# Kernel optimization log

Measured on AMD Instinct MI355X. Metric: run time of the kernel, lower is better.

Reference implementation:

```python
import jax, jax.numpy as jnp
import numpy as np

# static config (matches init_kwargs)
B, Q, D, H, L, P, V, T = 4, 32, 512, 8, 4, 4, 12000, 16
HD = D // H                      # attn_feat_dim = d_model / n_heads
TS = [2048, 1024, 512, 256]      # temporal_shapes (1-D feature pyramid)
LS = [0, 2048, 3072, 3584]       # level_start_index
S = sum(TS)


def setup_inputs() -> dict:
    key = jax.random.key(0)
    ks = jax.random.split(key, 20)
    f = jnp.float32
    def n(k, shape, s=0.02):
        return jax.random.normal(k, shape, dtype=f) * s
    return dict(
        seq_tokens=jax.random.randint(ks[0], (B * Q, T), 0, V),
        decoder_hidden_states=n(ks[1], (B, Q, D), 1.0),
        reference_points=jax.random.uniform(ks[2], (B, Q, 1), dtype=f),
        enc=n(ks[3], (B, S, D), 1.0),
        valid_ratios=jnp.ones((B, L), dtype=f),
        mask_flatten=jnp.zeros((B, S), dtype=bool),
        temporal_shapes=jnp.array(TS, dtype=jnp.int32),
        level_start_index=jnp.array(LS, dtype=jnp.int32),
        embed_W=jax.random.uniform(ks[4], (V, D), dtype=f, minval=-0.1, maxval=0.1),
        logit_W=jax.random.uniform(ks[5], (V, D), dtype=f, minval=-0.1, maxval=0.1),
        logit_b=jnp.zeros((V,), f),
        Wih=n(ks[6], (4 * D, 3 * D)),   # LSTM weight_ih (no bias), gate order i,f,g,o
        Whh=n(ks[7], (4 * D, D)),       # LSTM weight_hh
        value_W=n(ks[8], (D, D)), value_b=jnp.zeros((D,), f),
        off_W=n(ks[9], (H * L * P, 2 * D)), off_b=n(ks[10], (H * L * P,), 0.5),
        aw_W=n(ks[11], (H * L * P, 2 * D)), aw_b=jnp.zeros((H * L * P,), f),
        ctx_W=n(ks[12], (D, HD)), ctx_b=jnp.zeros((D,), f),
        hs_W=n(ks[13], (D, D)), hs_b=jnp.zeros((D,), f),
        alpha_W=n(ks[14], (1, D)), alpha_b=jnp.zeros((1,), f),
    )


def _forward(seq_tokens, decoder_hidden_states, reference_points, enc, valid_ratios,
             mask_flatten, temporal_shapes, level_start_index,
             embed_W, logit_W, logit_b, Wih, Whh, value_W, value_b,
             off_W, off_b, aw_W, aw_b, ctx_W, ctx_b, hs_W, hs_b, alpha_W, alpha_b):
    ts = [int(t) for t in np.asarray(temporal_shapes)]
    ls = [int(s) for s in np.asarray(level_start_index)]
    query = decoder_hidden_states            # (B, Q, D)
    BQ = B * Q
    # prepare_for_captioning: ref (B,Q,1) -> (B,Q,L,1) scaled by valid_ratios
    refp = reference_points[:, :, None, :] * valid_ratios[:, None, :, None]
    # value projection + padding mask
    value = jnp.where(mask_flatten[..., None], 0.0, enc @ value_W.T + value_b).reshape(B, S, H, HD)
    v_levels = [value[:, ls[l]:ls[l] + ts[l]].transpose(0, 2, 1, 3) for l in range(L)]  # (B,H,Tl,HD)
    ts_f = jnp.asarray(ts, dtype=query.dtype)

    def sample_level(v_l, loc, Tl):
        # 1-D linear interpolation, align_corners=False, zero padding (grid_sample style)
        # v_l: (B,H,Tl,HD); loc: (B,Q,H,P) normalized in [0,1]
        x = loc * Tl - 0.5
        x0 = jnp.floor(x)
        w = (x - x0)[..., None].transpose(0, 2, 1, 3, 4)   # (B,H,Q,P,1)
        i0 = x0.astype(jnp.int32)
        def gather(i):
            m = ((i >= 0) & (i < Tl))[..., None].astype(v_l.dtype).transpose(0, 2, 1, 3, 4)
            idx = jnp.clip(i, 0, Tl - 1).transpose(0, 2, 1, 3).reshape(B, H, Q * P)
            g = jnp.take_along_axis(v_l, idx[..., None], axis=2)  # (B,H,Q*P,HD)
            return g.reshape(B, H, Q, P, HD) * m
        return gather(i0) * (1.0 - w) + gather(i0 + 1) * w        # (B,H,Q,P,HD)

    def step(carry, tok):
        h, c = carry                                              # (BQ, D) each
        # TemporalMSDA query = cat(prev_h, query)
        hs_in = jnp.concatenate([h.reshape(B, Q, D), query], axis=2)       # (B,Q,2D)
        off = (hs_in @ off_W.T + off_b).reshape(B, Q, H, L, P)
        aw = jax.nn.softmax((hs_in @ aw_W.T + aw_b).reshape(B, Q, H, L * P), axis=-1)
        loc = refp[:, :, None, :, :] + off / ts_f[None, None, None, :, None]  # (B,Q,H,L,P)
        sampled = jnp.stack([sample_level(v_levels[l], loc[..., l, :], ts[l])
                             for l in range(L)], axis=3).reshape(B, H, Q, L * P, HD)
        weighted = sampled * aw.transpose(0, 2, 1, 3)[..., None]  # per-point MSDA-weighted values
        ctx = weighted.transpose(0, 2, 1, 3, 4).reshape(BQ, H, L * P, HD)
        # tanh additive attention over the L*P sampled points (per head)
        attn = ctx @ ctx_W.T + ctx_b                              # (BQ,H,LP,D)
        attn_h = (h @ hs_W.T + hs_b)[:, None, None, :]
        dot = (jnp.tanh(attn + attn_h) @ alpha_W.T + alpha_b)[..., 0]  # (BQ,H,LP)
        wgt = jax.nn.softmax(dot, axis=-1)
        attn_res = jnp.einsum('bhp,bhpd->bhd', wgt, ctx).reshape(BQ, D)
        # LSTM cell (bias=False), torch gate order i,f,g,o
        x = jnp.concatenate([embed_W[tok], attn_res, query.reshape(BQ, D)], axis=1)
        gates = x @ Wih.T + h @ Whh.T
        gi, gf, gg, go = jnp.split(gates, 4, axis=1)
        c2 = jax.nn.sigmoid(gf) * c + jax.nn.sigmoid(gi) * jnp.tanh(gg)
        h2 = jax.nn.sigmoid(go) * jnp.tanh(c2)
        return (h2, c2), jax.nn.log_softmax(h2 @ logit_W.T + logit_b, axis=-1)

    h0 = jnp.zeros((BQ, D), dtype=query.dtype)
    _, outs = jax.lax.scan(step, (h0, h0), seq_tokens[:, :-1].T)   # (T-1, BQ, V)
    return outs.transpose(1, 0, 2).reshape(B, Q, T - 1, V)


def reference(seq_tokens, decoder_hidden_states, reference_points, enc, valid_ratios,
              mask_flatten, temporal_shapes, level_start_index,
              embed_W, logit_W, logit_b, Wih, Whh, value_W, value_b,
              off_W, off_b, aw_W, aw_b, ctx_W, ctx_b, hs_W, hs_b, alpha_W, alpha_b):
    return _forward(seq_tokens, decoder_hidden_states, reference_points, enc, valid_ratios,
                    mask_flatten, temporal_shapes, level_start_index,
                    embed_W, logit_W, logit_b, Wih, Whh, value_W, value_b,
                    off_W, off_b, aw_W, aw_b, ctx_W, ctx_b, hs_W, hs_b, alpha_W, alpha_b)
```

## Files before the change

kernel.cpp:

```cpp
#include <hip/hip_runtime.h>

#define B_ 4
#define Q_ 32
#define D_ 512
#define H_ 8
#define L_ 4
#define P_ 4
#define V_ 12000
#define T_ 16
#define HD_ 64
#define S_ 3840
#define BQ_ 128
#define NSTEP 15
#define NSLAB 94

typedef __attribute__((ext_vector_type(8))) short short8;
typedef __attribute__((ext_vector_type(4))) float f32x4;

__device__ inline unsigned short f2bf(float x) {
  union { float f; unsigned u; } v; v.f = x;
  unsigned u = v.u;
  unsigned r = (u + 0x7fffu + ((u >> 16) & 1u)) >> 16;
  return (unsigned short)r;
}
__device__ inline float bf2f(unsigned short b) {
  union { unsigned u; float f; } v; v.u = ((unsigned)b) << 16; return v.f;
}
__device__ inline float fast_tanh(float x) {
  x = fminf(fmaxf(x, -15.f), 15.f);
  float e = __expf(2.f * x);
  return (e - 1.f) / (e + 1.f);
}
__device__ inline float sigmoidf_(float x) { return 1.f / (1.f + __expf(-x)); }

#define APAD 40
struct SmemGemm {
  unsigned short As0[128 * APAD], Bs0[128 * APAD];
  unsigned short As1[128 * APAD], Bs1[128 * APAD];
};
struct SmemGemmS {
  unsigned short As[128 * APAD], Bs[128 * APAD];
};
struct SmemSample {
  float ctx_s[16][HD_];
  unsigned short ctxbf[16][72];
  float aw_s[16];
  float wgt_s[16];
  float wred[4][16];
};

__device__ inline short8 cvt8(float4 v0, float4 v1) {
  short8 p;
  p[0] = (short)f2bf(v0.x); p[1] = (short)f2bf(v0.y);
  p[2] = (short)f2bf(v0.z); p[3] = (short)f2bf(v0.w);
  p[4] = (short)f2bf(v1.x); p[5] = (short)f2bf(v1.y);
  p[6] = (short)f2bf(v1.z); p[7] = (short)f2bf(v1.w);
  return p;
}

__device__ inline void mfma_step(const unsigned short* As, const unsigned short* Bs,
                                 f32x4 acc[4][4], int wm, int wn, int lane) {
  int r15 = lane & 15, koct = (lane >> 4) * 8;
  short8 a[4], b[4];
#pragma unroll
  for (int mf = 0; mf < 4; mf++)
    a[mf] = *(const short8*)(As + (wm * 64 + mf * 16 + r15) * APAD + koct);
#pragma unroll
  for (int nf = 0; nf < 4; nf++)
    b[nf] = *(const short8*)(Bs + (wn * 64 + nf * 16 + r15) * APAD + koct);
#pragma unroll
  for (int mf = 0; mf < 4; mf++)
#pragma unroll
    for (int nf = 0; nf < 4; nf++)
      acc[mf][nf] = __builtin_amdgcn_mfma_f32_16x16x32_bf16(a[mf], b[nf], acc[mf][nf], 0, 0, 0);
}

template <int NT, class FA, class FB>
__device__ inline void gemm_pipe(FA loadA, FB loadB, SmemGemm& sm,
                                 f32x4 acc[4][4], int wm, int wn, int lane, int tid) {
  int r = tid >> 2, ko = (tid & 3) * 8;
  short8 a0, a1, b0, b1;
  loadA(0, a0, a1); loadB(0, b0, b1);
#pragma unroll
  for (int t = 0; t < NT; t++) {
    unsigned short* As = (t & 1) ? sm.As1 : sm.As0;
    unsigned short* Bs = (t & 1) ? sm.Bs1 : sm.Bs0;
    *(short8*)(As + r * APAD + ko) = a0;
    *(short8*)(As + (r + 64) * APAD + ko) = a1;
    *(short8*)(Bs + r * APAD + ko) = b0;
    *(short8*)(Bs + (r + 64) * APAD + ko) = b1;
    short8 na0, na1, nb0, nb1;
    if (t + 1 < NT) { loadA(t + 1, na0, na1); loadB(t + 1, nb0, nb1); }
    __syncthreads();
    mfma_step(As, Bs, acc, wm, wn, lane);
    if (t + 1 < NT) { a0 = na0; a1 = na1; b0 = nb0; b1 = nb1; }
  }
}

template <int NT, class FA, class FB>
__device__ inline void gemm_simple(FA loadA, FB loadB, SmemGemmS& sm,
                                   f32x4 acc[4][4], int wm, int wn, int lane, int tid) {
  int r = tid >> 2, ko = (tid & 3) * 8;
#pragma unroll 2
  for (int t = 0; t < NT; t++) {
    short8 a0, a1, b0, b1;
    loadA(t, a0, a1); loadB(t, b0, b1);
    *(short8*)(sm.As + r * APAD + ko) = a0;
    *(short8*)(sm.As + (r + 64) * APAD + ko) = a1;
    *(short8*)(sm.Bs + r * APAD + ko) = b0;
    *(short8*)(sm.Bs + (r + 64) * APAD + ko) = b1;
    __syncthreads();
    mfma_step(sm.As, sm.Bs, acc, wm, wn, lane);
    __syncthreads();
  }
}

__device__ inline void mfma_epilogue(float* __restrict__ out, int ldo, int m0, int n0,
                                     int Nmax, const float* __restrict__ bias,
                                     const unsigned char* __restrict__ mask,
                                     const float* __restrict__ base,
                                     f32x4 acc[4][4], int wm, int wn, int lane) {
  int rb = (lane >> 4) * 4, cb = lane & 15;
#pragma unroll
  for (int nf = 0; nf < 4; nf++) {
    int col = n0 + wn * 64 + nf * 16 + cb;
    if (col >= Nmax) continue;
    float bv = bias ? bias[col] : 0.f;
#pragma unroll
    for (int mf = 0; mf < 4; mf++) {
#pragma unroll
      for (int j = 0; j < 4; j++) {
        int row = m0 + wm * 64 + mf * 16 + rb + j;
        float v = acc[mf][nf][j] + bv;
        if (base) v += base[(size_t)row * ldo + col];
        if (mask && mask[row]) v = 0.f;
        out[(size_t)row * ldo + col] = v;
      }
    }
  }
}

__device__ inline void mfma_epilogue_bf16b(unsigned short* __restrict__ out, int ldo,
                                           int m0, int n0,
                                           const float* __restrict__ bias,
                                           const unsigned char* __restrict__ mask,
                                           f32x4 acc[4][4], int wm, int wn, int lane) {
  int rb = (lane >> 4) * 4, cb = lane & 15;
#pragma unroll
  for (int nf = 0; nf < 4; nf++) {
    int col = n0 + wn * 64 + nf * 16 + cb;
    float bv = bias ? bias[col] : 0.f;
#pragma unroll
    for (int mf = 0; mf < 4; mf++) {
#pragma unroll
      for (int j = 0; j < 4; j++) {
        int row = m0 + wm * 64 + mf * 16 + rb + j;
        float v = acc[mf][nf][j] + bv;
        if (mask && mask[row]) v = 0.f;
        out[(size_t)row * ldo + col] = f2bf(v);
      }
    }
  }
}

__device__ inline void mfma_epilogue_bf16(unsigned short* __restrict__ out, int ldo, int n0,
                                          f32x4 acc[4][4], int wm, int wn, int lane) {
  int rb = (lane >> 4) * 4, cb = lane & 15;
#pragma unroll
  for (int nf = 0; nf < 4; nf++) {
    int col = n0 + wn * 64 + nf * 16 + cb;
#pragma unroll
    for (int mf = 0; mf < 4; mf++) {
#pragma unroll
      for (int j = 0; j < 4; j++) {
        int row = wm * 64 + mf * 16 + rb + j;
        out[(size_t)row * ldo + col] = f2bf(acc[mf][nf][j]);
      }
    }
  }
}

#define ACC_INIT f32x4 acc[4][4]; { f32x4 z = {0.f,0.f,0.f,0.f}; \
  _Pragma("unroll") for (int i_=0;i_<4;i_++) _Pragma("unroll") for (int j_=0;j_<4;j_++) acc[i_][j_]=z; }


__global__ __launch_bounds__(256) void k_prep(const float* __restrict__ logitW,
    const float* __restrict__ Wih, const float* __restrict__ Whh,
    const float* __restrict__ offW, const float* __restrict__ awW,
    const float* __restrict__ hsW, const float* __restrict__ valueW,
    const float* __restrict__ query, const float* __restrict__ ctxW,
    const int* __restrict__ seq, const float* __restrict__ embedW,
    unsigned short* __restrict__ logitWbf, unsigned short* __restrict__ Wihbf,
    unsigned short* __restrict__ Whhbf, unsigned short* __restrict__ offWbf,
    unsigned short* __restrict__ awWbf, unsigned short* __restrict__ hsWbf,
    unsigned short* __restrict__ valueWbf, unsigned short* __restrict__ qbf,
    unsigned short* __restrict__ ctxWbf, unsigned short* __restrict__ hall,
    float* __restrict__ c0, unsigned short* __restrict__ xembbf) {
  int gi = blockIdx.x * 256 + threadIdx.x;
  const int e0 = 1536000, e1 = e0 + 786432, e2 = e1 + 262144, e3 = e2 + 32768,
            e4 = e3 + 32768, e5 = e4 + 65536, e6 = e5 + 65536, e7 = e6 + 16384;
  const int e8 = e7 + 16384, e9 = e8 + 8192, e10 = e9 + 245760;
  if (gi < e7) {
    const float* src; unsigned short* dst; int lo, dsti;
    if (gi < e0)      { src = logitW; dst = logitWbf; lo = gi; dsti = lo; }
    else if (gi < e1) {
      src = Wih; dst = Wihbf; lo = gi - e0;
      int row = lo / 384, c4 = lo - row * 384;
      int g = row >> 9, d = row & 511, n = d >> 5, rr = d & 31;
      dsti = (n * 128 + g * 32 + rr) * 384 + c4;
    }
    else if (gi < e2) {
      src = Whh; dst = Whhbf; lo = gi - e1;
      int row = lo >> 7, c4 = lo & 127;
      int g = row >> 9, d = row & 511, n = d >> 5, rr = d & 31;
      dsti = (n * 128 + g * 32 + rr) * 128 + c4;
    }
    else if (gi < e3) { src = offW;   dst = offWbf;   lo = gi - e2; dsti = lo; }
    else if (gi < e4) { src = awW;    dst = awWbf;    lo = gi - e3; dsti = lo; }
    else if (gi < e5) { src = hsW;    dst = hsWbf;    lo = gi - e4; dsti = lo; }
    else if (gi < e6) { src = valueW; dst = valueWbf; lo = gi - e5; dsti = lo; }
    else              { src = query;  dst = qbf;      lo = gi - e6; dsti = lo; }
    float4 v = ((const float4*)src)[lo];
    ushort4 o;
    o.x = f2bf(v.x); o.y = f2bf(v.y); o.z = f2bf(v.z); o.w = f2bf(v.w);
    ((ushort4*)dst)[dsti] = o;
  } else if (gi < e8) {
    int i = gi - e7;
    ushort4 z4; z4.x = 0; z4.y = 0; z4.z = 0; z4.w = 0;
    ((ushort4*)hall)[i] = z4;
    float4 z = {0.f, 0.f, 0.f, 0.f};
    ((float4*)c0)[i] = z;
  } else if (gi < e9) {
    int i = gi - e8;
    float4 v = ((const float4*)ctxW)[i];
    ushort4 o;
    o.x = f2bf(v.x); o.y = f2bf(v.y); o.z = f2bf(v.z); o.w = f2bf(v.w);
    ((ushort4*)ctxWbf)[i] = o;
  } else if (gi < e10) {
    int i = gi - e9;
    int row = i >> 7, d4 = i & 127;
    int t = row >> 7, bq = row & 127;
    int tok = seq[bq * T_ + t];
    float4 v = ((const float4*)embedW)[(size_t)tok * 128 + d4];
    ushort4 o;
    o.x = f2bf(v.x); o.y = f2bf(v.y); o.z = f2bf(v.z); o.w = f2bf(v.w);
    ((ushort4*)xembbf)[(size_t)row * 128 + d4] = o;
  }
}

__global__ __launch_bounds__(256) void k_value(const float* __restrict__ enc,
    const unsigned short* __restrict__ valueWbf, const float* __restrict__ valueb,
    const unsigned char* __restrict__ mask, unsigned short* __restrict__ value) {
  __shared__ SmemGemmS sm;
  int blk = blockIdx.x;
  int xcd = blk & 7, j = blk >> 3;
  int m0 = (xcd * 15 + (j >> 2)) * 128, n0 = (j & 3) * 128;
  int tid = threadIdx.x;
  int lane = tid & 63, w = tid >> 6, wm = w >> 1, wn = w & 1;
  int r = tid >> 2, ko = (tid & 3) * 8;
  ACC_INIT;
  gemm_simple<16>(
    [&](int t, short8& x, short8& y) {
      const float4* s0 = (const float4*)(enc + (size_t)(m0 + r) * 512 + t * 32 + ko);
      const float4* s1 = (const float4*)(enc + (size_t)(m0 + r + 64) * 512 + t * 32 + ko);
      x = cvt8(s0[0], s0[1]); y = cvt8(s1[0], s1[1]);
    },
    [&](int t, short8& x, short8& y) {
      x = *(const short8*)(valueWbf + (size_t)(n0 + r) * 512 + t * 32 + ko);
      y = *(const short8*)(valueWbf + (size_t)(n0 + r + 64) * 512 + t * 32 + ko);
    },
    sm, acc, wm, wn, lane, tid);
  mfma_epilogue_bf16b(value, 512, m0, n0, valueb, mask, acc, wm, wn, lane);
}

__global__ __launch_bounds__(256) void k_qg(const unsigned short* __restrict__ qbf,
    const unsigned short* __restrict__ offWbf, const float* __restrict__ offb,
    const unsigned short* __restrict__ awWbf, const float* __restrict__ awb,
    float* __restrict__ off_base, float* __restrict__ aw_base,
    const unsigned short* __restrict__ xembbf,
    const unsigned short* __restrict__ Wihbf, unsigned short* __restrict__ gates_base) {
  __shared__ SmemGemmS sm;
  int blk = blockIdx.x;
  int tid = threadIdx.x;
  int lane = tid & 63, w = tid >> 6, wm = w >> 1, wn = w & 1;
  int r = tid >> 2, ko = (tid & 3) * 8;
  if (blk < 2) {
    const unsigned short* Bw = blk ? awWbf : offWbf;
    const float* bias = blk ? awb : offb;
    float* out = blk ? aw_base : off_base;
    ACC_INIT;
    gemm_simple<16>(
      [&](int t, short8& x, short8& y) {
        x = *(const short8*)(qbf + (size_t)r * 512 + t * 32 + ko);
        y = *(const short8*)(qbf + (size_t)(r + 64) * 512 + t * 32 + ko);
      },
      [&](int t, short8& x, short8& y) {
        x = *(const short8*)(Bw + (size_t)r * 1024 + 512 + t * 32 + ko);
        y = *(const short8*)(Bw + (size_t)(r + 64) * 1024 + 512 + t * 32 + ko);
      },
      sm, acc, wm, wn, lane, tid);
    mfma_epilogue(out, 128, 0, 0, 128, bias, nullptr, nullptr, acc, wm, wn, lane);
  } else {
    int g = blk - 2;
    int xcd = g & 7, j = g >> 3;
    int n0 = (xcd * 2 + (j >= 15)) * 128;
    int st = (j >= 15) ? (j - 15) : j;
    const unsigned short* xa = xembbf + (size_t)(st * 128) * 512;
    ACC_INIT;
    gemm_simple<32>(
      [&](int t, short8& x, short8& y) {
        const unsigned short* src = (t < 16) ? xa : qbf;
        int kk = (t < 16) ? t * 32 : (t - 16) * 32;
        x = *(const short8*)(src + (size_t)r * 512 + kk + ko);
        y = *(const short8*)(src + (size_t)(r + 64) * 512 + kk + ko);
      },
      [&](int t, short8& x, short8& y) {
        int kk = (t < 16) ? t * 32 : 1024 + (t - 16) * 32;
        x = *(const short8*)(Wihbf + (size_t)(n0 + r) * 1536 + kk + ko);
        y = *(const short8*)(Wihbf + (size_t)(n0 + r + 64) * 1536 + kk + ko);
      },
      sm, acc, wm, wn, lane, tid);
    mfma_epilogue_bf16(gates_base + (size_t)st * 128 * 2048, 2048, n0, acc, wm, wn, lane);
  }
}

__global__ __launch_bounds__(256) void k_sample(const unsigned short* __restrict__ value,
    const float* __restrict__ off_src, const float* __restrict__ aw_src,
    const float* __restrict__ hp_src, int hstride,
    const float* __restrict__ refp, const float* __restrict__ vrat,
    const unsigned short* __restrict__ ctxWbf, const float* __restrict__ ctxb,
    const float* __restrict__ alphaW, const float* __restrict__ alphab,
    unsigned short* __restrict__ attnbf) {
  __shared__ SmemSample sm;
  int blk = blockIdx.x;
  int bq = blk >> 3, h = blk & 7;
  int b = bq >> 5;
  int tid = threadIdx.x;
  int lane = tid & 63, wid = tid >> 6;

  if (tid < 16) {
    float v = aw_src[bq * 128 + h * 16 + tid];
    float m = v;
#pragma unroll
    for (int o = 8; o; o >>= 1) m = fmaxf(m, __shfl_xor(m, o, 16));
    float e = __expf(v - m);
    float s = e;
#pragma unroll
    for (int o = 8; o; o >>= 1) s += __shfl_xor(s, o, 16);
    sm.aw_s[tid] = e / s;
  }
  __syncthreads();

  {
    const int TSv[4] = {2048, 1024, 512, 256};
    const int LSv[4] = {0, 2048, 3072, 3584};
    float ref = refp[bq];
    int hd = tid & 63;
#pragma unroll
    for (int pp = 0; pp < 4; pp++) {
      int p = pp * 4 + (tid >> 6);
      int l = p >> 2;
      int Tl = TSv[l];
      float off = off_src[bq * 128 + h * 16 + p];
      float loc = ref * vrat[b * L_ + l] + off / (float)Tl;
      float x = loc * (float)Tl - 0.5f;
      float x0 = floorf(x);
      float wf = x - x0;
      int i0 = (int)x0;
      const unsigned short* vb = value + ((size_t)(b * S_ + LSv[l]) * D_) + h * HD_ + hd;
      float v0 = (i0 >= 0 && i0 < Tl) ? bf2f(vb[(size_t)i0 * D_]) : 0.f;
      float v1 = (i0 + 1 >= 0 && i0 + 1 < Tl) ? bf2f(vb[(size_t)(i0 + 1) * D_]) : 0.f;
      float cv = (v0 * (1.f - wf) + v1 * wf) * sm.aw_s[p];
      sm.ctx_s[p][hd] = cv;
      sm.ctxbf[p][hd] = f2bf(cv);
    }
  }
  __syncthreads();

  {
    int r15 = lane & 15, koct = (lane >> 4) * 8;
    int rb = (lane >> 4) * 4, cb = lane & 15;
    short8 a0 = *(const short8*)(&sm.ctxbf[r15][koct]);
    short8 a1 = *(const short8*)(&sm.ctxbf[r15][32 + koct]);
    float part0 = 0.f, part1 = 0.f, part2 = 0.f, part3 = 0.f;
#pragma unroll
    for (int nf = 0; nf < 8; nf++) {
      int d0 = wid * 128 + nf * 16;
      const unsigned short* bp = ctxWbf + (size_t)(d0 + r15) * 64;
      short8 b0 = *(const short8*)(bp + koct);
      short8 b1 = *(const short8*)(bp + 32 + koct);
      f32x4 acc = {0.f, 0.f, 0.f, 0.f};
      acc = __builtin_amdgcn_mfma_f32_16x16x32_bf16(a0, b0, acc, 0, 0, 0);
      acc = __builtin_amdgcn_mfma_f32_16x16x32_bf16(a1, b1, acc, 0, 0, 0);
      int d = d0 + cb;
      float add = ctxb[d] + hp_src[(size_t)hstride * bq + d];
      float al = alphaW[d];
      part0 += al * fast_tanh(acc[0] + add);
      part1 += al * fast_tanh(acc[1] + add);
      part2 += al * fast_tanh(acc[2] + add);
      part3 += al * fast_tanh(acc[3] + add);
    }
#pragma unroll
    for (int o = 8; o; o >>= 1) {
      part0 += __shfl_xor(part0, o, 16);
      part1 += __shfl_xor(part1, o, 16);
      part2 += __shfl_xor(part2, o, 16);
      part3 += __shfl_xor(part3, o, 16);
    }
    if (cb == 0) {
      sm.wred[wid][rb + 0] = part0;
      sm.wred[wid][rb + 1] = part1;
      sm.wred[wid][rb + 2] = part2;
      sm.wred[wid][rb + 3] = part3;
    }
  }
  __syncthreads();
  if (tid < 16) {
    float v = sm.wred[0][tid] + sm.wred[1][tid] + sm.wred[2][tid] + sm.wred[3][tid] + alphab[0];
    float m = v;
#pragma unroll
    for (int o = 8; o; o >>= 1) m = fmaxf(m, __shfl_xor(m, o, 16));
    float e = __expf(v - m);
    float s = e;
#pragma unroll
    for (int o = 8; o; o >>= 1) s += __shfl_xor(s, o, 16);
    sm.wgt_s[tid] = e / s;
  }
  __syncthreads();
  if (tid < 64) {
    float a = 0.f;
#pragma unroll
    for (int pi = 0; pi < 16; pi++) a += sm.wgt_s[pi] * sm.ctx_s[pi][tid];
    attnbf[bq * D_ + h * HD_ + tid] = f2bf(a);
  }
}

__global__ __launch_bounds__(256) void k_lstm_gemm(
    const unsigned short* __restrict__ attnbf, const unsigned short* __restrict__ hcur,
    const unsigned short* __restrict__ Wihbf, const unsigned short* __restrict__ Whhbf,
    float* __restrict__ gpart) {
  __shared__ SmemGemm sm;
  int tid = threadIdx.x;
  int lane = tid & 63, w = tid >> 6, wm = w >> 1, wn = w & 1;
  int r = tid >> 2, ko = (tid & 3) * 8;
  int n0 = blockIdx.x * 128;
  int kc = blockIdx.y;
  const unsigned short* Asrc = (kc < 2) ? (attnbf + kc * 256) : (hcur + (kc - 2) * 256);
  const unsigned short* Bsrc = (kc < 2) ? (Wihbf + (size_t)n0 * 1536 + 512 + kc * 256)
                                        : (Whhbf + (size_t)n0 * 512 + (kc - 2) * 256);
  int ldB = (kc < 2) ? 1536 : 512;
  ACC_INIT;
  gemm_pipe<8>(
    [&](int t, short8& x, short8& y) {
      x = *(const short8*)(Asrc + (size_t)r * 512 + t * 32 + ko);
      y = *(const short8*)(Asrc + (size_t)(r + 64) * 512 + t * 32 + ko);
    },
    [&](int t, short8& x, short8& y) {
      x = *(const short8*)(Bsrc + (size_t)r * ldB + t * 32 + ko);
      y = *(const short8*)(Bsrc + (size_t)(r + 64) * ldB + t * 32 + ko);
    },
    sm, acc, wm, wn, lane, tid);
  mfma_epilogue(gpart + (size_t)kc * 262144, 2048, 0, n0, 2048,
                nullptr, nullptr, nullptr, acc, wm, wn, lane);
}

__global__ __launch_bounds__(256) void k_cell(const float* __restrict__ gpart,
    const unsigned short* __restrict__ gbase_t,
    const float* __restrict__ c, float* __restrict__ cn, unsigned short* __restrict__ hout) {
  int idx = blockIdx.x * 256 + threadIdx.x;
  int bq = idx >> 9, d = idx & 511;
  int n = d >> 5, rr = d & 31;
  size_t rowoff = (size_t)bq * 2048 + n * 128 + rr;
  float g4[4];
#pragma unroll
  for (int gate = 0; gate < 4; gate++) {
    size_t off = rowoff + gate * 32;
    float s = bf2f(gbase_t[off]);
    s += gpart[off] + gpart[262144 + off] + gpart[2 * 262144 + off] + gpart[3 * 262144 + off];
    g4[gate] = s;
  }
  float cc = c[idx];
  float c2 = sigmoidf_(g4[1]) * cc + sigmoidf_(g4[0]) * fast_tanh(g4[2]);
  float h2 = sigmoidf_(g4[3]) * fast_tanh(c2);
  cn[idx] = c2;
  hout[idx] = f2bf(h2);
}

__global__ __launch_bounds__(256) void k_pre(const unsigned short* __restrict__ hbf,
    const unsigned short* __restrict__ offWbf, const unsigned short* __restrict__ awWbf,
    const unsigned short* __restrict__ hsWbf, const float* __restrict__ hsb,
    const float* __restrict__ off_base, const float* __restrict__ aw_base,
    float* __restrict__ offo, float* __restrict__ awo, float* __restrict__ hpo) {
  __shared__ SmemGemm sm;
  int blk = blockIdx.x;
  const unsigned short* Bw; const float* bias; const float* base;
  float* out; int ldkB, n0, ldo;
  if (blk == 0)      { Bw = offWbf; bias = nullptr; base = off_base; out = offo; ldkB = 1024; n0 = 0; ldo = 128; }
  else if (blk == 1) { Bw = awWbf;  bias = nullptr; base = aw_base;  out = awo;  ldkB = 1024; n0 = 0; ldo = 128; }
  else { Bw = hsWbf; bias = hsb; base = nullptr; out = hpo; ldkB = 512; n0 = (blk - 2) * 128; ldo = 512; }
  int tid = threadIdx.x;
  int lane = tid & 63, w = tid >> 6, wm = w >> 1, wn = w & 1;
  int r = tid >> 2, ko = (tid & 3) * 8;
  ACC_INIT;
  gemm_pipe<16>(
    [&](int t, short8& x, short8& y) {
      x = *(const short8*)(hbf + (size_t)r * 512 + t * 32 + ko);
      y = *(const short8*)(hbf + (size_t)(r + 64) * 512 + t * 32 + ko);
    },
    [&](int t, short8& x, short8& y) {
      x = *(const short8*)(Bw + (size_t)(n0 + r) * ldkB + t * 32 + ko);
      y = *(const short8*)(Bw + (size_t)(n0 + r + 64) * ldkB + t * 32 + ko);
    },
    sm, acc, wm, wn, lane, tid);
  mfma_epilogue(out, ldo, 0, n0, ldo, bias, nullptr, base, acc, wm, wn, lane);
}

__global__ __launch_bounds__(256) void k_logits_big(
    const unsigned short* __restrict__ logitWbf, const float* __restrict__ logitb,
    const unsigned short* __restrict__ hall, float* __restrict__ outp,
    float* __restrict__ m_sb, float* __restrict__ s_sb) {
  __shared__ SmemGemm sm;
  __shared__ float mred[128][2], sred[128][2];
  int blk = blockIdx.x;
  int swz = (blk & 7) * 177 + (blk >> 3);
  if (swz >= NSLAB * NSTEP) return;
  int slab = swz / NSTEP, t = swz % NSTEP;
  int n0 = slab * 128;
  int tid = threadIdx.x;
  int lane = tid & 63, w = tid >> 6, wm = w >> 1, wn = w & 1;
  int r = tid >> 2, ko = (tid & 3) * 8;
  const unsigned short* hn = hall + (size_t)(t + 1) * 65536;
  bool ok0 = (n0 + r) < V_, ok1 = (n0 + r + 64) < V_;
  ACC_INIT;
  gemm_pipe<16>(
    [&](int tt, short8& x, short8& y) {
      x = *(const short8*)(hn + (size_t)r * 512 + tt * 32 + ko);
      y = *(const short8*)(hn + (size_t)(r + 64) * 512 + tt * 32 + ko);
    },
    [&](int tt, short8& x, short8& y) {
      short8 z = {0, 0, 0, 0, 0, 0, 0, 0};
      x = ok0 ? *(const short8*)(logitWbf + (size_t)(n0 + r) * 512 + tt * 32 + ko) : z;
      y = ok1 ? *(const short8*)(logitWbf + (size_t)(n0 + r + 64) * 512 + tt * 32 + ko) : z;
    },
    sm, acc, wm, wn, lane, tid);
  int rb = (lane >> 4) * 4, cb = lane & 15;
#pragma unroll
  for (int mf = 0; mf < 4; mf++) {
#pragma unroll
    for (int j = 0; j < 4; j++) {
      int row = wm * 64 + mf * 16 + rb + j;
      float vv[4];
      float mx = -3.4e38f;
#pragma unroll
      for (int nf = 0; nf < 4; nf++) {
        int col = n0 + wn * 64 + nf * 16 + cb;
        bool ok = col < V_;
        float v = ok ? (acc[mf][nf][j] + logitb[col]) : -3.4e38f;
        if (ok) outp[((size_t)row * NSTEP + t) * V_ + col] = v;
        vv[nf] = v;
        mx = fmaxf(mx, v);
      }
#pragma unroll
      for (int o = 8; o; o >>= 1) mx = fmaxf(mx, __shfl_xor(mx, o, 16));
      float sme = 0.f;
#pragma unroll
      for (int nf = 0; nf < 4; nf++) sme += (vv[nf] > -3.0e38f) ? __expf(vv[nf] - mx) : 0.f;
#pragma unroll
      for (int o = 8; o; o >>= 1) sme += __shfl_xor(sme, o, 16);
      if (cb == 0) { mred[row][wn] = mx; sred[row][wn] = sme; }
    }
  }
  __syncthreads();
  if (tid < 128) {
    float m0 = mred[tid][0], m1 = mred[tid][1];
    float M = fmaxf(m0, m1);
    float Ssum = sred[tid][0] * __expf(m0 - M) + sred[tid][1] * __expf(m1 - M);
    m_sb[((size_t)t * 128 + tid) * 96 + slab] = M;
    s_sb[((size_t)t * 128 + tid) * 96 + slab] = Ssum;
  }
}

__global__ __launch_bounds__(256) void k_out_all(const float* __restrict__ m_sb,
    const float* __restrict__ s_sb, float* __restrict__ outp) {
  __shared__ float ms[NSLAB], ss[NSLAB];
  __shared__ float lse_s;
  int blk = blockIdx.x;
  int t = blk >> 7, row = blk & 127;
  int tid = threadIdx.x;
  size_t pbase = ((size_t)t * 128 + row) * 96;
  if (tid < NSLAB) { ms[tid] = m_sb[pbase + tid]; ss[tid] = s_sb[pbase + tid]; }
  __syncthreads();
  if (tid < 64) {
    float m = -3.4e38f, s = 0.f;
    for (int i = tid; i < NSLAB; i += 64) {
      float mi = ms[i], si = ss[i];
      float M = fmaxf(m, mi);
      s = s * __expf(m - M) + si * __expf(mi - M);
      m = M;
    }
#pragma unroll
    for (int o = 32; o; o >>= 1) {
      float mo = __shfl_xor(m, o, 64), so = __shfl_xor(s, o, 64);
      float M = fmaxf(m, mo);
      s = s * __expf(m - M) + so * __expf(mo - M);
      m = M;
    }
    if (tid == 0) lse_s = m + __logf(s);
  }
  __syncthreads();
  float lse = lse_s;
  float4* op = (float4*)(outp + ((size_t)row * NSTEP + t) * V_);
  for (int i = tid; i < V_ / 4; i += 256) {
    float4 v = op[i];
    v.x -= lse; v.y -= lse; v.z -= lse; v.w -= lse;
    op[i] = v;
  }
}

extern "C" void kernel_launch(void* const* d_in, const int* in_sizes, int n_in,
                              void* d_out, int out_size, void* d_ws, size_t ws_size,
                              hipStream_t stream) {
  const int* seq             = (const int*)d_in[0];
  const float* query         = (const float*)d_in[1];
  const float* refp          = (const float*)d_in[2];
  const float* enc           = (const float*)d_in[3];
  const float* vrat          = (const float*)d_in[4];
  const unsigned char* mask  = (const unsigned char*)d_in[5];
  const float* embedW        = (const float*)d_in[8];
  const float* logitW        = (const float*)d_in[9];
  const float* logitb        = (const float*)d_in[10];
  const float* Wih           = (const float*)d_in[11];
  const float* Whh           = (const float*)d_in[12];
  const float* valueW        = (const float*)d_in[13];
  const float* valueb        = (const float*)d_in[14];
  const float* offW          = (const float*)d_in[15];
  const float* offb          = (const float*)d_in[16];
  const float* awW           = (const float*)d_in[17];
  const float* awb           = (const float*)d_in[18];
  const float* ctxW          = (const float*)d_in[19];
  const float* ctxb          = (const float*)d_in[20];
  const float* hsW           = (const float*)d_in[21];
  const float* hsb           = (const float*)d_in[22];
  const float* alphaW        = (const float*)d_in[23];
  const float* alphab        = (const float*)d_in[24];

  char* wp = (char*)d_ws;
  auto alloc_f = [&](size_t n) { float* p = (float*)wp; wp += ((n * 4 + 255) / 256) * 256; return p; };
  auto alloc_u = [&](size_t n) { unsigned short* p = (unsigned short*)wp; wp += ((n * 2 + 255) / 256) * 256; return p; };

  float* gpart   = alloc_f((size_t)4 * BQ_ * 2048);
  float* hproj   = alloc_f((size_t)BQ_ * D_);
  float* offo    = alloc_f((size_t)BQ_ * 128);
  float* awo     = alloc_f((size_t)BQ_ * 128);
  float* off_base= alloc_f((size_t)BQ_ * 128);
  float* aw_base = alloc_f((size_t)BQ_ * 128);
  float* c0      = alloc_f((size_t)BQ_ * D_);
  float* c1      = alloc_f((size_t)BQ_ * D_);
  float* m_sb    = alloc_f((size_t)NSTEP * BQ_ * 96);
  float* s_sb    = alloc_f((size_t)NSTEP * BQ_ * 96);
  unsigned short* value   = alloc_u((size_t)B_ * S_ * D_);
  unsigned short* hall    = alloc_u((size_t)(NSTEP + 1) * BQ_ * D_);
  unsigned short* attnbf  = alloc_u((size_t)BQ_ * D_);
  unsigned short* qbf     = alloc_u((size_t)BQ_ * D_);
  unsigned short* ctxWbf  = alloc_u((size_t)512 * 64);
  unsigned short* xembbf  = alloc_u((size_t)NSTEP * BQ_ * D_);
  unsigned short* gates_base = alloc_u((size_t)NSTEP * BQ_ * 2048);
  unsigned short* logitWbf = alloc_u((size_t)V_ * D_);
  unsigned short* Wihbf    = alloc_u((size_t)2048 * 1536);
  unsigned short* Whhbf    = alloc_u((size_t)2048 * 512);
  unsigned short* offWbf   = alloc_u((size_t)128 * 1024);
  unsigned short* awWbf    = alloc_u((size_t)128 * 1024);
  unsigned short* hsWbf    = alloc_u((size_t)512 * 512);
  unsigned short* valueWbf = alloc_u((size_t)512 * 512);

  k_prep<<<11984, 256, 0, stream>>>(logitW, Wih, Whh, offW, awW, hsW, valueW, query, ctxW,
                                    seq, embedW,
                                    logitWbf, Wihbf, Whhbf, offWbf, awWbf, hsWbf,
                                    valueWbf, qbf, ctxWbf, hall, c0, xembbf);
  k_value<<<480, 256, 0, stream>>>(enc, valueWbf, valueb, mask, value);
  k_qg<<<242, 256, 0, stream>>>(qbf, offWbf, offb, awWbf, awb, off_base, aw_base,
                                xembbf, Wihbf, gates_base);

  float* cb[2] = {c0, c1};
  float* outp = (float*)d_out;

  for (int t = 0; t < NSTEP; t++) {
    const unsigned short* hcur = hall + (size_t)t * BQ_ * D_;
    unsigned short* hnxt = hall + (size_t)(t + 1) * BQ_ * D_;
    if (t == 0)
      k_sample<<<1024, 256, 0, stream>>>(value, off_base, aw_base, hsb, 0, refp, vrat,
                                         ctxWbf, ctxb, alphaW, alphab, attnbf);
    else
      k_sample<<<1024, 256, 0, stream>>>(value, offo, awo, hproj, 512, refp, vrat,
                                         ctxWbf, ctxb, alphaW, alphab, attnbf);
    k_lstm_gemm<<<dim3(16, 4), 256, 0, stream>>>(attnbf, hcur, Wihbf, Whhbf, gpart);
    k_cell<<<256, 256, 0, stream>>>(gpart, gates_base + (size_t)t * BQ_ * 2048,
                                    cb[t & 1], cb[(t + 1) & 1], hnxt);
    if (t + 1 < NSTEP)
      k_pre<<<6, 256, 0, stream>>>(hnxt, offWbf, awWbf, hsWbf, hsb,
                                   off_base, aw_base, offo, awo, hproj);
  }

  k_logits_big<<<1416, 256, 0, stream>>>(logitWbf, logitb, hall, outp, m_sb, s_sb);
  k_out_all<<<NSTEP * BQ_, 256, 0, stream>>>(m_sb, s_sb, outp);
}
```

Measured before the change: 762.1 us.

## Retile logits GEMM to 256x128 tiles spanning all timesteps

The logits kernel now treats all 15 timesteps' hidden states as one 1920-row M dimension and computes 256x128 output tiles instead of 128x128 tiles per timestep. This halves the block count and doubles reuse of each loaded logit_W tile, cutting repeated weight reads from global memory. In exchange it drops the previous pipelined gemm_pipe helper for a simple two-barrier load/compute loop with more accumulator registers, which may lower occupancy and expose load latency.

```diff
diff --git a/kernel.cpp b/kernel.cpp
--- a/kernel.cpp
+++ b/kernel.cpp
@@ -519,44 +519,80 @@
     const unsigned short* __restrict__ logitWbf, const float* __restrict__ logitb,
     const unsigned short* __restrict__ hall, float* __restrict__ outp,
     float* __restrict__ m_sb, float* __restrict__ s_sb) {
-  __shared__ SmemGemm sm;
-  __shared__ float mred[128][2], sred[128][2];
+  __shared__ unsigned short As[256 * APAD];
+  __shared__ unsigned short Bs[128 * APAD];
+  __shared__ float mred[256][2], sred[256][2];
   int blk = blockIdx.x;
-  int swz = (blk & 7) * 177 + (blk >> 3);
-  if (swz >= NSLAB * NSTEP) return;
-  int slab = swz / NSTEP, t = swz % NSTEP;
+  int swz = (blk & 7) * 94 + (blk >> 3);
+  int slab = swz >> 3, mt = swz & 7;
   int n0 = slab * 128;
+  int gm0 = mt * 256;
   int tid = threadIdx.x;
   int lane = tid & 63, w = tid >> 6, wm = w >> 1, wn = w & 1;
-  int r = tid >> 2, ko = (tid & 3) * 8;
-  const unsigned short* hn = hall + (size_t)(t + 1) * 65536;
-  bool ok0 = (n0 + r) < V_, ok1 = (n0 + r + 64) < V_;
-  ACC_INIT;
-  gemm_pipe<16>(
-    [&](int tt, short8& x, short8& y) {
-      x = *(const short8*)(hn + (size_t)r * 512 + tt * 32 + ko);
-      y = *(const short8*)(hn + (size_t)(r + 64) * 512 + tt * 32 + ko);
-    },
-    [&](int tt, short8& x, short8& y) {
-      short8 z = {0, 0, 0, 0, 0, 0, 0, 0};
-      x = ok0 ? *(const short8*)(logitWbf + (size_t)(n0 + r) * 512 + tt * 32 + ko) : z;
-      y = ok1 ? *(const short8*)(logitWbf + (size_t)(n0 + r + 64) * 512 + tt * 32 + ko) : z;
-    },
-    sm, acc, wm, wn, lane, tid);
+  int r15 = lane & 15, koct = (lane >> 4) * 8;
+
+  f32x4 acc[8][4];
+  { f32x4 z = {0.f, 0.f, 0.f, 0.f};
+#pragma unroll
+    for (int i = 0; i < 8; i++)
+#pragma unroll
+      for (int j = 0; j < 4; j++) acc[i][j] = z; }
+
+#pragma unroll 2
+  for (int kt = 0; kt < 16; kt++) {
+#pragma unroll
+    for (int i = 0; i < 4; i++) {
+      int slot = i * 256 + tid;
+      int r = slot >> 2, k8 = (slot & 3) * 8;
+      short8 v = {0, 0, 0, 0, 0, 0, 0, 0};
+      int gr = gm0 + r;
+      if (gr < 1920) {
+        int tt = gr >> 7, row = gr & 127;
+        v = *(const short8*)(hall + (size_t)(tt + 1) * 65536 + (size_t)row * 512 + kt * 32 + k8);
+      }
+      *(short8*)(As + r * APAD + k8) = v;
+    }
+#pragma unroll
+    for (int i = 0; i < 2; i++) {
+      int slot = i * 256 + tid;
+      int r = slot >> 2, k8 = (slot & 3) * 8;
+      short8 v = {0, 0, 0, 0, 0, 0, 0, 0};
+      if (n0 + r < V_) v = *(const short8*)(logitWbf + (size_t)(n0 + r) * 512 + kt * 32 + k8);
+      *(short8*)(Bs + r * APAD + k8) = v;
+    }
+    __syncthreads();
+    short8 a[8], b[4];
+#pragma unroll
+    for (int mf = 0; mf < 8; mf++)
+      a[mf] = *(const short8*)(As + (wm * 128 + mf * 16 + r15) * APAD + koct);
+#pragma unroll
+    for (int nf = 0; nf < 4; nf++)
+      b[nf] = *(const short8*)(Bs + (wn * 64 + nf * 16 + r15) * APAD + koct);
+#pragma unroll
+    for (int mf = 0; mf < 8; mf++)
+#pragma unroll
+      for (int nf = 0; nf < 4; nf++)
+        acc[mf][nf] = __builtin_amdgcn_mfma_f32_16x16x32_bf16(a[mf], b[nf], acc[mf][nf], 0, 0, 0);
+    __syncthreads();
+  }
+
   int rb = (lane >> 4) * 4, cb = lane & 15;
 #pragma unroll
-  for (int mf = 0; mf < 4; mf++) {
+  for (int mf = 0; mf < 8; mf++) {
 #pragma unroll
     for (int j = 0; j < 4; j++) {
-      int row = wm * 64 + mf * 16 + rb + j;
+      int lr = wm * 128 + mf * 16 + rb + j;
+      int gr = gm0 + lr;
+      bool rok = gr < 1920;
+      int tt = gr >> 7, row = gr & 127;
       float vv[4];
       float mx = -3.4e38f;
 #pragma unroll
       for (int nf = 0; nf < 4; nf++) {
         int col = n0 + wn * 64 + nf * 16 + cb;
-        bool ok = col < V_;
+        bool ok = rok && (col < V_);
         float v = ok ? (acc[mf][nf][j] + logitb[col]) : -3.4e38f;
-        if (ok) outp[((size_t)row * NSTEP + t) * V_ + col] = v;
+        if (ok) outp[((size_t)row * NSTEP + tt) * V_ + col] = v;
         vv[nf] = v;
         mx = fmaxf(mx, v);
       }
@@ -567,16 +603,21 @@
       for (int nf = 0; nf < 4; nf++) sme += (vv[nf] > -3.0e38f) ? __expf(vv[nf] - mx) : 0.f;
 #pragma unroll
       for (int o = 8; o; o >>= 1) sme += __shfl_xor(sme, o, 16);
-      if (cb == 0) { mred[row][wn] = mx; sred[row][wn] = sme; }
+      if (cb == 0) { mred[lr][wn] = mx; sred[lr][wn] = sme; }
     }
   }
   __syncthreads();
-  if (tid < 128) {
-    float m0 = mred[tid][0], m1 = mred[tid][1];
-    float M = fmaxf(m0, m1);
-    float Ssum = sred[tid][0] * __expf(m0 - M) + sred[tid][1] * __expf(m1 - M);
-    m_sb[((size_t)t * 128 + tid) * 96 + slab] = M;
-    s_sb[((size_t)t * 128 + tid) * 96 + slab] = Ssum;
+  {
+    int lr = tid;
+    int gr = gm0 + lr;
+    if (gr < 1920) {
+      float m0 = mred[lr][0], m1 = mred[lr][1];
+      float M = fmaxf(m0, m1);
+      float Ssum = sred[lr][0] * __expf(m0 - M) + sred[lr][1] * __expf(m1 - M);
+      int tt = gr >> 7, row = gr & 127;
+      m_sb[((size_t)tt * 128 + row) * 96 + slab] = M;
+      s_sb[((size_t)tt * 128 + row) * 96 + slab] = Ssum;
+    }
   }
 }
 
@@ -701,6 +742,6 @@
                                    off_base, aw_base, offo, awo, hproj);
   }
 
-  k_logits_big<<<1416, 256, 0, stream>>>(logitWbf, logitb, hall, outp, m_sb, s_sb);
+  k_logits_big<<<752, 256, 0, stream>>>(logitWbf, logitb, hall, outp, m_sb, s_sb);
   k_out_all<<<NSTEP * BQ_, 256, 0, stream>>>(m_sb, s_sb, outp);
 }
```

New measurement: 869.3 us. 1.14x slower.
